# Performance work log

Hardware: AMD Instinct MI355X
Metric: run time of the kernel (lower is better)

## Reference

```python
import jax, jax.numpy as jnp
import numpy as np

D_MODEL = 1024
N_HEADS = 16
HEAD_DIM = D_MODEL // N_HEADS
ROPE_THETA = 10000.0
EPS = 1e-6


def _split_qkv(qkv, h):
    b, n, _ = qkv.shape
    qkv = qkv.reshape(b, n, 3, h, -1)          # b n three h d
    qkv = jnp.transpose(qkv, (2, 0, 3, 1, 4))  # three b h n d
    return qkv[0], qkv[1], qkv[2]


def _rms_norm(x, scale):
    # RMSNorm over head dim with learnable per-dim scale (QKNorm)
    var = jnp.mean(jnp.square(x), axis=-1, keepdims=True)
    return x * jax.lax.rsqrt(var + EPS) * scale


def _rope(x, pos):
    # x: [b, h, n, d], pos: [n] float; rotate-half RoPE
    d = x.shape[-1]
    inv_freq = 1.0 / (ROPE_THETA ** (jnp.arange(0, d, 2, dtype=jnp.float32) / d))
    ang = pos[:, None] * inv_freq[None, :]                 # [n, d/2]
    cos = jnp.cos(ang)[None, None]                          # [1,1,n,d/2]
    sin = jnp.sin(ang)[None, None]
    x1 = x[..., 0::2]
    x2 = x[..., 1::2]
    r1 = x1 * cos - x2 * sin
    r2 = x1 * sin + x2 * cos
    return jnp.stack([r1, r2], axis=-1).reshape(x.shape)


def setup_inputs() -> dict:
    key = jax.random.key(0)
    ks = jax.random.split(key, 16)
    d = D_MODEL
    s = 0.02
    inp = {
        "x_1": jax.random.normal(ks[0], (2, 1536, d), dtype=jnp.float32),
        "x_2": jax.random.normal(ks[1], (2, 512, d), dtype=jnp.float32),
        "W_qkv1": jax.random.normal(ks[2], (3 * d, d), dtype=jnp.float32) * s,
        "b_qkv1": jnp.zeros((3 * d,), dtype=jnp.float32),
        "W_qkv2": jax.random.normal(ks[3], (3 * d, d), dtype=jnp.float32) * s,
        "b_qkv2": jnp.zeros((3 * d,), dtype=jnp.float32),
        "W_out1": jax.random.normal(ks[4], (d, d), dtype=jnp.float32) * s,
        "b_out1": jnp.zeros((d,), dtype=jnp.float32),
        "W_out2": jax.random.normal(ks[5], (d, d), dtype=jnp.float32) * s,
        "b_out2": jnp.zeros((d,), dtype=jnp.float32),
        "q_scale1": jnp.ones((HEAD_DIM,), dtype=jnp.float32),
        "k_scale1": jnp.ones((HEAD_DIM,), dtype=jnp.float32),
        "q_scale2": jnp.ones((HEAD_DIM,), dtype=jnp.float32),
        "k_scale2": jnp.ones((HEAD_DIM,), dtype=jnp.float32),
    }
    return inp


def reference(x_1, x_2, W_qkv1, b_qkv1, W_qkv2, b_qkv2,
              W_out1, b_out1, W_out2, b_out2,
              q_scale1, k_scale1, q_scale2, k_scale2):
    b, n1, d = x_1.shape
    n2 = x_2.shape[1]
    h = N_HEADS

    q1, k1, v1 = _split_qkv(x_1 @ W_qkv1.T + b_qkv1, h)
    q2, k2, v2 = _split_qkv(x_2 @ W_qkv2.T + b_qkv2, h)

    q1 = _rms_norm(q1, q_scale1); k1 = _rms_norm(k1, k_scale1)
    q2 = _rms_norm(q2, q_scale2); k2 = _rms_norm(k2, k_scale2)

    # AVRoPE: stream-1 tokens at positions [0, n1), stream-2 continues at [n1, n1+n2)
    pos1 = jnp.arange(n1, dtype=jnp.float32)
    pos2 = n1 + jnp.arange(n2, dtype=jnp.float32)
    q1 = _rope(q1, pos1); q2 = _rope(q2, pos2)
    k1 = _rope(k1, pos1); k2 = _rope(k2, pos2)

    q = jnp.concatenate([q1, q2], axis=-2)   # [b,h,N,dh]
    k = jnp.concatenate([k1, k2], axis=-2)
    v = jnp.concatenate([v1, v2], axis=-2)

    scale = 1.0 / jnp.sqrt(jnp.asarray(q.shape[-1], dtype=q.dtype))
    scores = jnp.einsum('bhqd,bhkd->bhqk', q, k) * scale
    attn = jax.nn.softmax(scores, axis=-1)
    x = jnp.einsum('bhqk,bhkd->bhqd', attn, v)      # [b,h,N,dh]

    x = jnp.transpose(x, (0, 2, 1, 3)).reshape(b, n1 + n2, d)  # merge heads

    out1 = x[:, :n1] @ W_out1.T + b_out1
    out2 = x[:, n1:] @ W_out2.T + b_out2
    return out1, out2
```

## Files before the change

### kernel.cpp

```cpp
#include <hip/hip_runtime.h>
#include <hip/hip_bf16.h>
#include <math.h>

#define D_MODEL 1024
#define N_HEADS 16
#define HEAD_DIM 64
#define SEQ1 1536
#define SEQ2 512
#define NTOT 2048
#define BATCH 2

typedef __attribute__((ext_vector_type(8))) short bf16x8;
typedef __attribute__((ext_vector_type(4))) float f32x4;

__device__ __forceinline__ unsigned short f2bf(float f) {
  unsigned u = __builtin_bit_cast(unsigned, f);
  u += 0x7FFFu + ((u >> 16) & 1u);
  return (unsigned short)(u >> 16);
}
__device__ __forceinline__ float bf2f(unsigned short h) {
  unsigned u = ((unsigned)h) << 16;
  return __builtin_bit_cast(float, u);
}

__device__ __forceinline__ void gload16(const void* g, void* l) {
  __builtin_amdgcn_global_load_lds(
      (const __attribute__((address_space(1))) void*)g,
      (__attribute__((address_space(3))) void*)l, 16, 0, 0);
}

struct CvtArgs {
  const float* src[6];
  unsigned short* dst[6];
  int prefix[7];
};

__global__ __launch_bounds__(256) void cvt_all(CvtArgs a)
{
  int e = (blockIdx.x * 256 + threadIdx.x) * 4;
  if (e >= a.prefix[6]) return;
  int s = 0;
#pragma unroll
  for (int i = 1; i < 6; ++i) s += (e >= a.prefix[i]) ? 1 : 0;
  int lo = e - a.prefix[s];
  float4 v = *(const float4*)(a.src[s] + lo);
  ushort4 o;
  o.x = f2bf(v.x); o.y = f2bf(v.y); o.z = f2bf(v.z); o.w = f2bf(v.w);
  *(ushort4*)(a.dst[s] + lo) = o;
}

struct GemmSeg {
  const unsigned short* A;
  const unsigned short* W;
  const float* bias;
  void* C;
  int N, K, tilesX;
};

template <int WRITE_BF16>
__global__ __launch_bounds__(256) void gemm2(GemmSeg g0, GemmSeg g1, int tiles0)
{
  __shared__ __align__(16) unsigned short Alds[128 * 64];
  __shared__ __align__(16) unsigned short Blds[128 * 64];
  const int id = blockIdx.x;
  const bool in1 = (id >= tiles0);
  const unsigned short* A = in1 ? g1.A : g0.A;
  const unsigned short* W = in1 ? g1.W : g0.W;
  const float* bias = in1 ? g1.bias : g0.bias;
  void* Cv = in1 ? g1.C : g0.C;
  const int N = in1 ? g1.N : g0.N;
  const int K = in1 ? g1.K : g0.K;
  const int tilesX = in1 ? g1.tilesX : g0.tilesX;
  const int lid = in1 ? id - tiles0 : id;
  const int m0 = (lid / tilesX) * 128, n0 = (lid % tilesX) * 128;

  const int tid = threadIdx.x;
  const int lane = tid & 63, wave = tid >> 6;
  const int wm = wave >> 1, wn = wave & 1;
  const int l15 = lane & 15, l4 = lane >> 4;

  f32x4 acc[4][4];
#pragma unroll
  for (int m = 0; m < 4; ++m)
#pragma unroll
    for (int n = 0; n < 4; ++n)
#pragma unroll
      for (int r = 0; r < 4; ++r) acc[m][n][r] = 0.0f;

  for (int k0 = 0; k0 < K; k0 += 64) {
    __syncthreads();
#pragma unroll
    for (int c = 0; c < 4; ++c) {
      int off = c * 4096 + tid * 16;
      int row = off >> 7;
      int c16g = ((off & 127) >> 4) ^ (row & 7);
      int dstb = c * 4096 + (tid >> 6) * 1024;
      gload16(A + (size_t)(m0 + row) * K + k0 + c16g * 8, (char*)Alds + dstb);
      gload16(W + (size_t)(n0 + row) * K + k0 + c16g * 8, (char*)Blds + dstb);
    }
    __syncthreads();
#pragma unroll
    for (int kk = 0; kk < 2; ++kk) {
      bf16x8 af[4], bfr[4];
#pragma unroll
      for (int m = 0; m < 4; ++m) {
        int r = wm * 64 + m * 16 + l15;
        int colb = (kk * 64 + l4 * 16) ^ ((r & 7) << 4);
        af[m] = *(const bf16x8*)((const char*)Alds + r * 128 + colb);
      }
#pragma unroll
      for (int n = 0; n < 4; ++n) {
        int r = wn * 64 + n * 16 + l15;
        int colb = (kk * 64 + l4 * 16) ^ ((r & 7) << 4);
        bfr[n] = *(const bf16x8*)((const char*)Blds + r * 128 + colb);
      }
#pragma unroll
      for (int m = 0; m < 4; ++m)
#pragma unroll
        for (int n = 0; n < 4; ++n)
          acc[m][n] = __builtin_amdgcn_mfma_f32_16x16x32_bf16(
              af[m], bfr[n], acc[m][n], 0, 0, 0);
    }
  }

#pragma unroll
  for (int m = 0; m < 4; ++m)
#pragma unroll
    for (int n = 0; n < 4; ++n)
#pragma unroll
      for (int r = 0; r < 4; ++r) {
        int row = m0 + wm * 64 + m * 16 + l4 * 4 + r;
        int col = n0 + wn * 64 + n * 16 + l15;
        float v = acc[m][n][r] + bias[col];
        if (WRITE_BF16)
          ((unsigned short*)Cv)[(size_t)row * N + col] = f2bf(v);
        else
          ((float*)Cv)[(size_t)row * N + col] = v;
      }
}

__global__ __launch_bounds__(256) void qkv_transform(
    const unsigned short* __restrict__ qkv1,
    const unsigned short* __restrict__ qkv2,
    const float* __restrict__ qs1, const float* __restrict__ ks1,
    const float* __restrict__ qs2, const float* __restrict__ ks2,
    unsigned short* __restrict__ qO, unsigned short* __restrict__ kO,
    unsigned short* __restrict__ vO)
{
  const int row = blockIdx.x;
  const int lane = threadIdx.x & 63;
  const int wave = threadIdx.x >> 6;
  const float QSCALE = 0.18033688011112042f;

  const unsigned short* src;
  const float* qs;
  const float* ks;
  int b, pos;
  if (row < BATCH * SEQ1) {
    b = row / SEQ1;
    pos = row % SEQ1;
    src = qkv1 + (size_t)row * (3 * D_MODEL);
    qs = qs1; ks = ks1;
  } else {
    int r2 = row - BATCH * SEQ1;
    b = r2 / SEQ2;
    pos = SEQ1 + (r2 % SEQ2);
    src = qkv2 + (size_t)r2 * (3 * D_MODEL);
    qs = qs2; ks = ks2;
  }

  const int j = lane >> 1;
  const float LOG2_THETA = 13.287712379549449f;
  float inv_freq = exp2f(-((float)(2 * j) / 64.0f) * LOG2_THETA);
  float ang = (float)pos * inv_freq;
  float sn, cs;
  sincosf(ang, &sn, &cs);

  for (int h = wave; h < N_HEADS; h += 4) {
    float xq = bf2f(src[0 * D_MODEL + h * HEAD_DIM + lane]);
    float xk = bf2f(src[1 * D_MODEL + h * HEAD_DIM + lane]);
    float xv = bf2f(src[2 * D_MODEL + h * HEAD_DIM + lane]);

    float sq = xq * xq, sk = xk * xk;
#pragma unroll
    for (int o = 32; o > 0; o >>= 1) {
      sq += __shfl_xor(sq, o);
      sk += __shfl_xor(sk, o);
    }
    float xqn = xq * rsqrtf(sq * (1.0f / 64.0f) + 1e-6f) * qs[lane];
    float xkn = xk * rsqrtf(sk * (1.0f / 64.0f) + 1e-6f) * ks[lane];

    float pq = __shfl_xor(xqn, 1);
    float pk = __shfl_xor(xkn, 1);
    float oq, ok;
    if (lane & 1) { oq = pq * sn + xqn * cs; ok = pk * sn + xkn * cs; }
    else          { oq = xqn * cs - pq * sn; ok = xkn * cs - pk * sn; }

    size_t o = (((size_t)b * N_HEADS + h) * NTOT + pos) * HEAD_DIM + lane;
    qO[o] = f2bf(oq * QSCALE);
    kO[o] = f2bf(ok);
    vO[o] = f2bf(xv);
  }
}

__global__ __launch_bounds__(256) void v_transpose(
    const unsigned short* __restrict__ v, unsigned short* __restrict__ vt)
{
  const int pt = blockIdx.x, bh = blockIdx.y;
  __shared__ unsigned short t[64][72];
  const int tid = threadIdx.x;
  const unsigned short* src = v + ((size_t)bh * NTOT + pt * 64) * 64;
#pragma unroll
  for (int c = 0; c < 2; ++c) {
    int off = c * 4096 + tid * 16;
    int row = off >> 7, c16 = (off & 127) >> 4;
    bf16x8 x = *(const bf16x8*)(src + row * 64 + c16 * 8);
#pragma unroll
    for (int j = 0; j < 8; ++j) t[row][c16 * 8 + j] = (unsigned short)x[j];
  }
  __syncthreads();
  unsigned short* dst = vt + (size_t)bh * 64 * NTOT + pt * 64;
#pragma unroll
  for (int c = 0; c < 2; ++c) {
    int off = c * 4096 + tid * 16;
    int d = off >> 7, p16 = (off & 127) >> 4;
    bf16x8 x;
#pragma unroll
    for (int j = 0; j < 8; ++j) x[j] = (short)t[p16 * 8 + j][d];
    *(bf16x8*)(dst + (size_t)d * NTOT + p16 * 8) = x;
  }
}

__global__ __launch_bounds__(256) void attn_mfma(
    const unsigned short* __restrict__ Qg, const unsigned short* __restrict__ Kg,
    const unsigned short* __restrict__ VTg,
    unsigned short* __restrict__ xb1, unsigned short* __restrict__ xb2)
{
  const int qt = blockIdx.x, bh = blockIdx.y;
  const int b = bh >> 4, h = bh & 15;
  const int tid = threadIdx.x, lane = tid & 63, w = tid >> 6;
  const int l15 = lane & 15, l4 = lane >> 4;

  __shared__ __align__(16) unsigned short Klds[2][64 * 64];
  __shared__ __align__(16) unsigned short Vlds[2][64 * 64];
  __shared__ __align__(16) unsigned short Plds[128 * 64];

  const size_t base = (size_t)bh * NTOT * HEAD_DIM;
  bf16x8 qf[2][2];
#pragma unroll
  for (int g = 0; g < 2; ++g) {
    const unsigned short* qp =
        Qg + base + (size_t)(qt * 128 + g * 64 + w * 16 + l15) * 64 + l4 * 8;
    qf[g][0] = *(const bf16x8*)qp;
    qf[g][1] = *(const bf16x8*)(qp + 32);
  }

  bf16x8 ones;
#pragma unroll
  for (int i = 0; i < 8; ++i) ones[i] = (short)0x3F80;

  f32x4 acc_o[2][4], acc_l[2];
  float m_run[2][4];
#pragma unroll
  for (int g = 0; g < 2; ++g) {
#pragma unroll
    for (int dt = 0; dt < 4; ++dt)
#pragma unroll
      for (int r = 0; r < 4; ++r) acc_o[g][dt][r] = 0.0f;
#pragma unroll
    for (int r = 0; r < 4; ++r) { acc_l[g][r] = 0.0f; m_run[g][r] = -1e30f; }
  }

  const unsigned short* kp = Kg + base;
  const unsigned short* vtp = VTg + (size_t)bh * HEAD_DIM * NTOT;

#define STAGE(bf, kt)                                                         \
  {                                                                           \
    _Pragma("unroll")                                                         \
    for (int c = 0; c < 2; ++c) {                                             \
      int off = c * 4096 + tid * 16;                                          \
      int row = off >> 7;                                                     \
      int c16g = ((off & 127) >> 4) ^ (row & 7);                              \
      int dstb = c * 4096 + (tid >> 6) * 1024;                                \
      gload16(kp + (size_t)((kt) * 64 + row) * 64 + c16g * 8,                 \
              (char*)Klds[bf] + dstb);                                        \
      gload16(vtp + (size_t)row * NTOT + (kt) * 64 + c16g * 8,                \
              (char*)Vlds[bf] + dstb);                                        \
    }                                                                         \
  }

  STAGE(0, 0);

  for (int kt = 0; kt < NTOT / 64; ++kt) {
    const int cur = kt & 1;
    __syncthreads();
    if (kt + 1 < NTOT / 64) STAGE(cur ^ 1, kt + 1);

    f32x4 sacc[2][4];
#pragma unroll
    for (int g = 0; g < 2; ++g)
#pragma unroll
      for (int ct = 0; ct < 4; ++ct)
#pragma unroll
        for (int r = 0; r < 4; ++r) sacc[g][ct][r] = 0.0f;
    __builtin_amdgcn_s_setprio(1);
#pragma unroll
    for (int kk = 0; kk < 2; ++kk) {
#pragma unroll
      for (int ct = 0; ct < 4; ++ct) {
        int r = ct * 16 + l15;
        int colb = (kk * 64 + l4 * 16) ^ ((r & 7) << 4);
        bf16x8 kf = *(const bf16x8*)((const char*)Klds[cur] + r * 128 + colb);
#pragma unroll
        for (int g = 0; g < 2; ++g)
          sacc[g][ct] = __builtin_amdgcn_mfma_f32_16x16x32_bf16(
              qf[g][kk], kf, sacc[g][ct], 0, 0, 0);
      }
    }
    __builtin_amdgcn_s_setprio(0);

#pragma unroll
    for (int g = 0; g < 2; ++g) {
#pragma unroll
      for (int r = 0; r < 4; ++r) {
        float tm = fmaxf(fmaxf(sacc[g][0][r], sacc[g][1][r]),
                         fmaxf(sacc[g][2][r], sacc[g][3][r]));
#pragma unroll
        for (int o = 1; o < 16; o <<= 1) tm = fmaxf(tm, __shfl_xor(tm, o));
        float mo = m_run[g][r];
        if (tm > mo + 8.0f) {
          float fac = exp2f(mo - tm);
          m_run[g][r] = tm;
#pragma unroll
          for (int dt = 0; dt < 4; ++dt) acc_o[g][dt][r] *= fac;
          acc_l[g][r] *= fac;
        }
        float mc = m_run[g][r];
        int row = g * 64 + w * 16 + l4 * 4 + r;
#pragma unroll
        for (int ct = 0; ct < 4; ++ct) {
          float pv = exp2f(sacc[g][ct][r] - mc);
          int colb = (ct * 32 + l15 * 2) ^ ((row & 7) << 4);
          *(unsigned short*)((char*)Plds + row * 128 + colb) = f2bf(pv);
        }
      }
    }

    __builtin_amdgcn_s_setprio(1);
#pragma unroll
    for (int ks = 0; ks < 2; ++ks) {
      bf16x8 pf[2];
#pragma unroll
      for (int g = 0; g < 2; ++g) {
        int pr = g * 64 + w * 16 + l15;
        int pcolb = (ks * 64 + l4 * 16) ^ ((pr & 7) << 4);
        pf[g] = *(const bf16x8*)((const char*)Plds + pr * 128 + pcolb);
      }
#pragma unroll
      for (int dt = 0; dt < 4; ++dt) {
        int vr = dt * 16 + l15;
        int vcolb = (ks * 64 + l4 * 16) ^ ((vr & 7) << 4);
        bf16x8 vf = *(const bf16x8*)((const char*)Vlds[cur] + vr * 128 + vcolb);
#pragma unroll
        for (int g = 0; g < 2; ++g)
          acc_o[g][dt] = __builtin_amdgcn_mfma_f32_16x16x32_bf16(
              pf[g], vf, acc_o[g][dt], 0, 0, 0);
      }
#pragma unroll
      for (int g = 0; g < 2; ++g)
        acc_l[g] = __builtin_amdgcn_mfma_f32_16x16x32_bf16(
            pf[g], ones, acc_l[g], 0, 0, 0);
    }
    __builtin_amdgcn_s_setprio(0);
  }
#undef STAGE

#pragma unroll
  for (int g = 0; g < 2; ++g)
#pragma unroll
    for (int r = 0; r < 4; ++r) {
      int n = qt * 128 + g * 64 + w * 16 + l4 * 4 + r;
      float inv = 1.0f / acc_l[g][r];
      unsigned short* dst;
      if (n < SEQ1) dst = xb1 + ((size_t)b * SEQ1 + n) * D_MODEL;
      else          dst = xb2 + ((size_t)b * SEQ2 + (n - SEQ1)) * D_MODEL;
#pragma unroll
      for (int dt = 0; dt < 4; ++dt)
        dst[h * 64 + dt * 16 + l15] = f2bf(acc_o[g][dt][r] * inv);
    }
}

extern "C" void kernel_launch(void* const* d_in, const int* in_sizes, int n_in,
                              void* d_out, int out_size, void* d_ws,
                              size_t ws_size, hipStream_t stream)
{
  (void)in_sizes; (void)n_in; (void)out_size; (void)ws_size;

  const float* x1  = (const float*)d_in[0];
  const float* x2  = (const float*)d_in[1];
  const float* Wq1 = (const float*)d_in[2];
  const float* bq1 = (const float*)d_in[3];
  const float* Wq2 = (const float*)d_in[4];
  const float* bq2 = (const float*)d_in[5];
  const float* Wo1 = (const float*)d_in[6];
  const float* bo1 = (const float*)d_in[7];
  const float* Wo2 = (const float*)d_in[8];
  const float* bo2 = (const float*)d_in[9];
  const float* qs1 = (const float*)d_in[10];
  const float* ks1 = (const float*)d_in[11];
  const float* qs2 = (const float*)d_in[12];
  const float* ks2 = (const float*)d_in[13];
  float* out = (float*)d_out;

  unsigned short* ws = (unsigned short*)d_ws;
  const size_t SX1 = (size_t)BATCH * SEQ1 * D_MODEL;
  const size_t SX2 = (size_t)BATCH * SEQ2 * D_MODEL;
  const size_t SW  = (size_t)3 * D_MODEL * D_MODEL;
  const size_t SWO = (size_t)D_MODEL * D_MODEL;
  const size_t SQ1 = (size_t)BATCH * SEQ1 * 3 * D_MODEL;
  const size_t SQ2 = (size_t)BATCH * SEQ2 * 3 * D_MODEL;
  const size_t SH  = (size_t)BATCH * N_HEADS * NTOT * HEAD_DIM;

  unsigned short* x1b  = ws;
  unsigned short* x2b  = x1b + SX1;
  unsigned short* Wq1b = x2b + SX2;
  unsigned short* Wq2b = Wq1b + SW;
  unsigned short* Wo1b = Wq2b + SW;
  unsigned short* Wo2b = Wo1b + SWO;
  unsigned short* qkv1 = Wo2b + SWO;
  unsigned short* qkv2 = qkv1 + SQ1;
  unsigned short* qb   = qkv2 + SQ2;
  unsigned short* kb   = qb + SH;
  unsigned short* vb   = kb + SH;
  unsigned short* vtb  = vb + SH;
  unsigned short* xb1  = vtb + SH;
  unsigned short* xb2  = xb1 + SX1;

  CvtArgs ca;
  ca.src[0] = x1;  ca.dst[0] = x1b;
  ca.src[1] = x2;  ca.dst[1] = x2b;
  ca.src[2] = Wq1; ca.dst[2] = Wq1b;
  ca.src[3] = Wq2; ca.dst[3] = Wq2b;
  ca.src[4] = Wo1; ca.dst[4] = Wo1b;
  ca.src[5] = Wo2; ca.dst[5] = Wo2b;
  ca.prefix[0] = 0;
  ca.prefix[1] = (int)SX1;
  ca.prefix[2] = (int)(SX1 + SX2);
  ca.prefix[3] = (int)(SX1 + SX2 + SW);
  ca.prefix[4] = (int)(SX1 + SX2 + 2 * SW);
  ca.prefix[5] = (int)(SX1 + SX2 + 2 * SW + SWO);
  ca.prefix[6] = (int)(SX1 + SX2 + 2 * SW + 2 * SWO);
  cvt_all<<<(ca.prefix[6] / 4 + 255) / 256, 256, 0, stream>>>(ca);

  {
    GemmSeg s0{x1b, Wq1b, bq1, qkv1, 3 * D_MODEL, D_MODEL, 3 * D_MODEL / 128};
    GemmSeg s1{x2b, Wq2b, bq2, qkv2, 3 * D_MODEL, D_MODEL, 3 * D_MODEL / 128};
    int t0 = (BATCH * SEQ1 / 128) * (3 * D_MODEL / 128);
    int t1 = (BATCH * SEQ2 / 128) * (3 * D_MODEL / 128);
    gemm2<1><<<t0 + t1, 256, 0, stream>>>(s0, s1, t0);
  }

  qkv_transform<<<BATCH * (SEQ1 + SEQ2), 256, 0, stream>>>(
      qkv1, qkv2, qs1, ks1, qs2, ks2, qb, kb, vb);

  v_transpose<<<dim3(NTOT / 64, BATCH * N_HEADS), 256, 0, stream>>>(vb, vtb);

  attn_mfma<<<dim3(NTOT / 128, BATCH * N_HEADS), 256, 0, stream>>>(
      qb, kb, vtb, xb1, xb2);

  {
    GemmSeg s0{xb1, Wo1b, bo1, out, D_MODEL, D_MODEL, D_MODEL / 128};
    GemmSeg s1{xb2, Wo2b, bo2, out + (size_t)BATCH * SEQ1 * D_MODEL,
               D_MODEL, D_MODEL, D_MODEL / 128};
    int t0 = (BATCH * SEQ1 / 128) * (D_MODEL / 128);
    int t1 = (BATCH * SEQ2 / 128) * (D_MODEL / 128);
    gemm2<0><<<t0 + t1, 256, 0, stream>>>(s0, s1, t0);
  }
}
```

Before: 312.6 us.

## Transpose QK^T MFMA so each lane owns one query row for softmax

Swaps the MFMA operands for the score product so the accumulator layout gives each lane a single query row across 16 key columns. Row max and row sum then need only two cross-lane shuffles instead of a 16-lane butterfly per row, and the row sum is accumulated in registers rather than through an extra MFMA against a ones vector. P is written to LDS as packed 8-byte stores instead of scalar 2-byte stores. The rescale decision becomes wave-uniform via __all, and correction factors are shuffled back to the output accumulator layout, which adds some shuffles in exchange.

New measurement: 291.3 us. 1.07x faster.

```diff
diff --git a/kernel.cpp b/kernel.cpp
--- a/kernel.cpp
+++ b/kernel.cpp
@@ -255,20 +255,16 @@
     qf[g][1] = *(const bf16x8*)(qp + 32);
   }
 
-  bf16x8 ones;
-#pragma unroll
-  for (int i = 0; i < 8; ++i) ones[i] = (short)0x3F80;
-
-  f32x4 acc_o[2][4], acc_l[2];
-  float m_run[2][4];
+  f32x4 acc_o[2][4];
+  float m_run[2], l_run[2];
 #pragma unroll
   for (int g = 0; g < 2; ++g) {
 #pragma unroll
     for (int dt = 0; dt < 4; ++dt)
 #pragma unroll
       for (int r = 0; r < 4; ++r) acc_o[g][dt][r] = 0.0f;
-#pragma unroll
-    for (int r = 0; r < 4; ++r) { acc_l[g][r] = 0.0f; m_run[g][r] = -1e30f; }
+    m_run[g] = -1e30f;
+    l_run[g] = 0.0f;
   }
 
   const unsigned short* kp = Kg + base;
@@ -314,36 +310,53 @@
 #pragma unroll
         for (int g = 0; g < 2; ++g)
           sacc[g][ct] = __builtin_amdgcn_mfma_f32_16x16x32_bf16(
-              qf[g][kk], kf, sacc[g][ct], 0, 0, 0);
+              kf, qf[g][kk], sacc[g][ct], 0, 0, 0);
       }
     }
     __builtin_amdgcn_s_setprio(0);
 
 #pragma unroll
     for (int g = 0; g < 2; ++g) {
-#pragma unroll
-      for (int r = 0; r < 4; ++r) {
-        float tm = fmaxf(fmaxf(sacc[g][0][r], sacc[g][1][r]),
-                         fmaxf(sacc[g][2][r], sacc[g][3][r]));
-#pragma unroll
-        for (int o = 1; o < 16; o <<= 1) tm = fmaxf(tm, __shfl_xor(tm, o));
-        float mo = m_run[g][r];
-        if (tm > mo + 8.0f) {
-          float fac = exp2f(mo - tm);
-          m_run[g][r] = tm;
-#pragma unroll
-          for (int dt = 0; dt < 4; ++dt) acc_o[g][dt][r] *= fac;
-          acc_l[g][r] *= fac;
+      float tm = fmaxf(fmaxf(sacc[g][0][0], sacc[g][0][1]),
+                       fmaxf(sacc[g][0][2], sacc[g][0][3]));
+#pragma unroll
+      for (int ct = 1; ct < 4; ++ct)
+        tm = fmaxf(tm, fmaxf(fmaxf(sacc[g][ct][0], sacc[g][ct][1]),
+                             fmaxf(sacc[g][ct][2], sacc[g][ct][3])));
+      tm = fmaxf(tm, __shfl_xor(tm, 16));
+      tm = fmaxf(tm, __shfl_xor(tm, 32));
+      float mo = m_run[g];
+      if (!__all(tm <= mo + 8.0f)) {
+        float mn = fmaxf(mo, tm);
+        float fac = exp2f(mo - mn);
+        m_run[g] = mn;
+        l_run[g] *= fac;
+#pragma unroll
+        for (int r = 0; r < 4; ++r) {
+          float fr = __shfl(fac, l4 * 4 + r);
+#pragma unroll
+          for (int dt = 0; dt < 4; ++dt) acc_o[g][dt][r] *= fr;
         }
-        float mc = m_run[g][r];
-        int row = g * 64 + w * 16 + l4 * 4 + r;
-#pragma unroll
-        for (int ct = 0; ct < 4; ++ct) {
-          float pv = exp2f(sacc[g][ct][r] - mc);
-          int colb = (ct * 32 + l15 * 2) ^ ((row & 7) << 4);
-          *(unsigned short*)((char*)Plds + row * 128 + colb) = f2bf(pv);
-        }
-      }
+      }
+      float mc = m_run[g];
+      float rs = 0.0f;
+      int qrow = g * 64 + w * 16 + l15;
+#pragma unroll
+      for (int ct = 0; ct < 4; ++ct) {
+        float p0 = exp2f(sacc[g][ct][0] - mc);
+        float p1 = exp2f(sacc[g][ct][1] - mc);
+        float p2 = exp2f(sacc[g][ct][2] - mc);
+        float p3 = exp2f(sacc[g][ct][3] - mc);
+        rs += (p0 + p1) + (p2 + p3);
+        uint2 pw;
+        pw.x = (unsigned)f2bf(p0) | ((unsigned)f2bf(p1) << 16);
+        pw.y = (unsigned)f2bf(p2) | ((unsigned)f2bf(p3) << 16);
+        *(uint2*)((char*)Plds + qrow * 128 +
+                  ((ct * 32 + l4 * 8) ^ ((qrow & 7) << 4))) = pw;
+      }
+      rs += __shfl_xor(rs, 16);
+      rs += __shfl_xor(rs, 32);
+      l_run[g] += rs;
     }
 
     __builtin_amdgcn_s_setprio(1);
@@ -366,28 +379,26 @@
           acc_o[g][dt] = __builtin_amdgcn_mfma_f32_16x16x32_bf16(
               pf[g], vf, acc_o[g][dt], 0, 0, 0);
       }
-#pragma unroll
-      for (int g = 0; g < 2; ++g)
-        acc_l[g] = __builtin_amdgcn_mfma_f32_16x16x32_bf16(
-            pf[g], ones, acc_l[g], 0, 0, 0);
     }
     __builtin_amdgcn_s_setprio(0);
   }
 #undef STAGE
 
 #pragma unroll
-  for (int g = 0; g < 2; ++g)
+  for (int g = 0; g < 2; ++g) {
+    float inv = 1.0f / l_run[g];
 #pragma unroll
     for (int r = 0; r < 4; ++r) {
+      float ir = __shfl(inv, l4 * 4 + r);
       int n = qt * 128 + g * 64 + w * 16 + l4 * 4 + r;
-      float inv = 1.0f / acc_l[g][r];
       unsigned short* dst;
       if (n < SEQ1) dst = xb1 + ((size_t)b * SEQ1 + n) * D_MODEL;
       else          dst = xb2 + ((size_t)b * SEQ2 + (n - SEQ1)) * D_MODEL;
 #pragma unroll
       for (int dt = 0; dt < 4; ++dt)
-        dst[h * 64 + dt * 16 + l15] = f2bf(acc_o[g][dt][r] * inv);
-    }
+        dst[h * 64 + dt * 16 + l15] = f2bf(acc_o[g][dt][r] * ir);
+    }
+  }
 }
 
 extern "C" void kernel_launch(void* const* d_in, const int* in_sizes, int n_in,
```
